# Optimization experiments

Measured on AMD Instinct MI355X. Metric: run time of the kernel, lower is better.

Reference implementation:

```python
import jax, jax.numpy as jnp
import numpy as np

N_SAMPLES = 131072
N_EVENTS = 128
N_ATOMS = 32
ATOM_SIZE = 512
LATENT_DIM = 16
TOTAL_LAYERS = 7  # log2(n_events)


def setup_inputs() -> dict:
    key = jax.random.key(0)
    ks = jax.random.split(key, 9)
    r = lambda k, s: jax.random.normal(k, s, dtype=jnp.float32) * 0.1
    return {
        "base_latent": r(ks[0], (1, LATENT_DIM)),
        "to_off_w": r(ks[1], (TOTAL_LAYERS, 2, LATENT_DIM)),
        "split_w": r(ks[2], (TOTAL_LAYERS, 2 * LATENT_DIM, LATENT_DIM)),
        "split_b": r(ks[3], (TOTAL_LAYERS, 2 * LATENT_DIM)),
        "atoms": r(ks[4], (N_ATOMS, ATOM_SIZE)),
        "to_atoms_w": r(ks[5], (N_ATOMS, LATENT_DIM)),
        "to_atoms_b": r(ks[6], (N_ATOMS,)),
        "to_amp_w": r(ks[7], (1, LATENT_DIM)),
        "to_amp_b": r(ks[8], (1,)),
    }


def fft_shift(a, shift):
    # FFT-based fractional delay: pad to 3*n, phase-rotate spectrum, crop.
    n = a.shape[-1]
    shift_samples = shift * n * 0.5  # shift: (B, E, 1)
    a = jnp.pad(a, [(0, 0)] * (a.ndim - 1) + [(0, n * 2)])
    spec = jnp.fft.rfft(a, axis=-1, norm="ortho")
    n_coeffs = spec.shape[-1]
    coeffs = (jnp.arange(n_coeffs) * 2j * jnp.pi) / n_coeffs  # (n_coeffs,)
    spec = spec * jnp.exp(coeffs * shift_samples)  # broadcast (B,E,n_coeffs)
    samples = jnp.fft.irfft(spec, axis=-1, norm="ortho")
    return samples[..., :n]


def _forward(base_latent, to_off_w, split_w, split_b, atoms,
             to_atoms_w, to_atoms_b, to_amp_w, to_amp_b):
    x = base_latent[:, None, :]                     # (1, 1, L)
    base_times = jnp.zeros((1, 1, 1), dtype=x.dtype)
    for i in range(TOTAL_LAYERS):
        scale = 1.0 / (2 ** i)
        b, e, _ = x.shape
        to = jax.nn.sigmoid(jnp.einsum("bel,ol->beo", x, to_off_w[i]))  # (b,e,2)
        base_times = (base_times + to * scale).reshape(b, e * 2, 1)
        split = jnp.einsum("bel,ol->beo", x, split_w[i]) + split_b[i]   # (b,e,2L)
        x = split.reshape(b, e * 2, LATENT_DIM)
    # x: (1, 128, L), base_times: (1, 128, 1)
    mix = jnp.einsum("bel,al->bea", x, to_atoms_w) + to_atoms_b          # (1,E,A)
    ev = jnp.einsum("bea,at->bet", mix, atoms)                           # (1,E,512)
    n_arr = jnp.arange(ATOM_SIZE, dtype=ev.dtype)
    window = 0.54 - 0.46 * jnp.cos(2.0 * jnp.pi * n_arr / ATOM_SIZE)     # periodic hamming
    ev = ev * window
    ev = jnp.pad(ev, ((0, 0), (0, 0), (0, N_SAMPLES - ATOM_SIZE)))       # (1,E,n_samples)
    ev = ev / (jnp.linalg.norm(ev, axis=-1, keepdims=True) + 1e-8)       # unit_norm
    amps = jnp.einsum("bel,ol->beo", x, to_amp_w) + to_amp_b             # (1,E,1)
    ev = ev * amps
    scheduled = fft_shift(ev, base_times)                                # (1,E,n_samples)
    return jnp.sum(scheduled, axis=1, keepdims=True)                     # (1,1,n_samples)


def reference(base_latent, to_off_w, split_w, split_b, atoms,
              to_atoms_w, to_atoms_b, to_amp_w, to_amp_b):
    return _forward(base_latent, to_off_w, split_w, split_b, atoms,
                    to_atoms_w, to_atoms_b, to_amp_w, to_amp_b)
```

## Files before the change

### kernel.cpp

```cpp
#include <hip/hip_runtime.h>
#include <hip/hip_bf16.h>
#include <math.h>

constexpr int NSAMP  = 131072;
constexpr int NEV    = 128;
constexpr int ASIZE  = 512;
constexpr int LDIM   = 16;
constexpr int NLAYER = 7;
constexpr int NFFT   = 393216;
constexpr int MHALF  = 196608;
constexpr int QN     = 65536;
constexpr double TWO_PI = 6.283185307179586;


__device__ __forceinline__ float2 cmulf(float2 a, float2 b) {
    return make_float2(a.x*b.x - a.y*b.y, a.x*b.y + a.y*b.x);
}
__device__ __forceinline__ float2 CADD(float2 a, float2 b){ return make_float2(a.x+b.x, a.y+b.y); }
__device__ __forceinline__ float2 CSUB(float2 a, float2 b){ return make_float2(a.x-b.x, a.y-b.y); }

__device__ __forceinline__ void phase_sc(float th32, float* ps, float* pc) {
    const double th = (double)th32;
    const double n  = rint(th * 0.15915494309189535);
    double r = fma(-n, 6.283185307179586, th);
    r = fma(-n, 2.4492935982947064e-16, r);
    __sincosf((float)r, ps, pc);
}

#define RT2 0.70710678118654752f
#define DFT8F(A0,A1,A2,A3,A4,A5,A6,A7, X0,X1,X2,X3,X4,X5,X6,X7) { \
  float2 b0=CADD(A0,A4), b1=CADD(A1,A5), b2=CADD(A2,A6), b3=CADD(A3,A7); \
  float2 c0=CSUB(A0,A4); \
  float2 d1=CSUB(A1,A5), d2=CSUB(A2,A6), d3=CSUB(A3,A7); \
  float2 c1=make_float2((d1.x+d1.y)*RT2, (d1.y-d1.x)*RT2); \
  float2 c2=make_float2(d2.y, -d2.x); \
  float2 c3=make_float2((d3.y-d3.x)*RT2, -(d3.x+d3.y)*RT2); \
  float2 t0=CADD(b0,b2), t1=CSUB(b0,b2), t2=CADD(b1,b3), t3=CSUB(b1,b3); \
  X0=CADD(t0,t2); X4=CSUB(t0,t2); \
  X2=make_float2(t1.x+t3.y, t1.y-t3.x); X6=make_float2(t1.x-t3.y, t1.y+t3.x); \
  t0=CADD(c0,c2); t1=CSUB(c0,c2); t2=CADD(c1,c3); t3=CSUB(c1,c3); \
  X1=CADD(t0,t2); X5=CSUB(t0,t2); \
  X3=make_float2(t1.x+t3.y, t1.y-t3.x); X7=make_float2(t1.x-t3.y, t1.y+t3.x); \
}

__global__ __launch_bounds__(256) void twiddles(
    double2* __restrict__ Tw256, double2* __restrict__ Tw512,
    double2* __restrict__ Tw768, double2* __restrict__ Tw64k)
{
    const int t = threadIdx.x;
    double s, c;
    sincos(TWO_PI*(double)t/256.0,   &s, &c); Tw256[t] = make_double2(c, s);
    sincos(TWO_PI*(double)t/512.0,   &s, &c); Tw512[t] = make_double2(c, s);
    sincos(TWO_PI*(double)t/768.0,   &s, &c); Tw768[t] = make_double2(c, s);
    sincos(TWO_PI*(double)t/65536.0, &s, &c); Tw64k[t] = make_double2(c, s);
}

__global__ __launch_bounds__(256) void tree_f32(
    const float* __restrict__ base, const float* __restrict__ to_off_w,
    const float* __restrict__ split_w, const float* __restrict__ split_b,
    float* __restrict__ xF, float* __restrict__ sF)
{
    __shared__ float xA[NEV*LDIM], xB[NEV*LDIM], bA[NEV], bB[NEV];
    const int tid = threadIdx.x;
    if (tid < LDIM) xA[tid] = base[tid];
    if (tid == 0) bA[0] = 0.0f;
    __syncthreads();
    float* xi = xA; float* xo = xB; float* bi = bA; float* bo = bB;
    for (int i = 0; i < NLAYER; ++i) {
        const int ein = 1 << i;
        const float scale = 1.0f / (float)(1 << i);
        for (int idx = tid; idx < ein*32; idx += 256) {
            const int ep = idx >> 5, o2 = idx & 31;
            const float* wr = split_w + (i*32 + o2)*LDIM;
            const float* xr = xi + ep*LDIM;
            float s = __fmul_rn(xr[0], wr[0]);
            for (int l = 1; l < LDIM; ++l)
                s = __fadd_rn(s, __fmul_rn(xr[l], wr[l]));
            s = __fadd_rn(s, split_b[i*32 + o2]);
            xo[(ep*2 + (o2>>4))*LDIM + (o2&15)] = s;
        }
        for (int idx = tid; idx < ein*2; idx += 256) {
            const int ep = idx >> 1, o = idx & 1;
            const float* wr = to_off_w + (i*2 + o)*LDIM;
            const float* xr = xi + ep*LDIM;
            float v = __fmul_rn(xr[0], wr[0]);
            for (int l = 1; l < LDIM; ++l)
                v = __fadd_rn(v, __fmul_rn(xr[l], wr[l]));
            const float ef = (float)exp(-(double)v);
            const float sg = __fdiv_rn(1.0f, __fadd_rn(1.0f, ef));
            bo[ep*2 + o] = __fadd_rn(bi[ep], __fmul_rn(sg, scale));
        }
        __syncthreads();
        float* t;
        t = xi; xi = xo; xo = t;
        t = bi; bi = bo; bo = t;
    }
    for (int idx = tid; idx < NEV*LDIM; idx += 256) xF[idx] = xi[idx];
    for (int e = tid; e < NEV; e += 256)
        sF[e] = __fmul_rn(__fmul_rn(bi[e], 131072.0f), 0.5f);
}

__global__ __launch_bounds__(256) void events_f32(
    const float* __restrict__ atoms, const float* __restrict__ to_atoms_w,
    const float* __restrict__ to_atoms_b, const float* __restrict__ to_amp_w,
    const float* __restrict__ to_amp_b, const float* __restrict__ xF,
    float* __restrict__ zf)
{
    const int e = blockIdx.x;
    const int tid = threadIdx.x;
    __shared__ float mixS[32];
    __shared__ float evS[ASIZE];
    __shared__ double red[256];
    __shared__ float scl[2];
    const float* x = xF + e*LDIM;
    if (tid < 32) {
        const float* wr = to_atoms_w + tid*LDIM;
        float m = __fmul_rn(x[0], wr[0]);
        for (int l = 1; l < LDIM; ++l) m = __fadd_rn(m, __fmul_rn(x[l], wr[l]));
        mixS[tid] = __fadd_rn(m, to_atoms_b[tid]);
    }
    __syncthreads();
    double ss = 0.0;
    for (int u = tid; u < ASIZE; u += 256) {
        float v = __fmul_rn(mixS[0], atoms[u]);
        for (int a = 1; a < 32; ++a)
            v = __fadd_rn(v, __fmul_rn(mixS[a], atoms[a*ASIZE + u]));
        const float ang = __fdiv_rn(__fmul_rn(6.283185307179586f, (float)u), 512.0f);
        const float cw = (float)cos((double)ang);
        const float w  = __fsub_rn(0.54f, __fmul_rn(0.46f, cw));
        v = __fmul_rn(v, w);
        evS[u] = v;
        ss += (double)v * (double)v;
    }
    red[tid] = ss; __syncthreads();
    for (int s = 128; s > 0; s >>= 1) { if (tid < s) red[tid] += red[tid+s]; __syncthreads(); }
    if (tid == 0) {
        const float nf = (float)sqrt(red[0]);
        scl[0] = __fadd_rn(nf, 1e-8f);
        float a = __fmul_rn(x[0], to_amp_w[0]);
        for (int l = 1; l < LDIM; ++l) a = __fadd_rn(a, __fmul_rn(x[l], to_amp_w[l]));
        scl[1] = __fadd_rn(a, to_amp_b[0]);
    }
    __syncthreads();
    const float den = scl[0], amp = scl[1];
    for (int u = tid; u < ASIZE; u += 256)
        zf[e*ASIZE + u] = __fmul_rn(__fdiv_rn(evS[u], den), amp);
}

__global__ __launch_bounds__(256, 4) void forward_reg8(
    const float* __restrict__ zf, const float* __restrict__ sF,
    float* __restrict__ Hqf)
{
    __shared__ float2 FB[4*576];
    __shared__ float2 T[512];
    __shared__ float2 W[448];
    __shared__ float  sSh[32];
    const int b       = blockIdx.x >> 2;
    const int quarter = blockIdx.x & 3;
    const int tid  = threadIdx.x;
    const int wave = tid >> 6, lane = tid & 63;
    float2* F = FB + wave*576;
    const int e0 = quarter*32;

    for (int j = tid; j < 512; j += 256) {
        double s1, c1;
        sincos(-TWO_PI*(double)(b*j)/(double)NFFT, &s1, &c1);
        T[j] = make_float2((float)c1, (float)s1);
        if (j < 448) {
            sincos(-TWO_PI*(double)j/512.0, &s1, &c1);
            W[j] = make_float2((float)c1, (float)s1);
        }
    }
    if (tid < 32) sSh[tid] = sF[e0 + tid];
    __syncthreads();

    float c2a[4], c2b[4];
    #pragma unroll
    for (int j = 0; j < 4; ++j) {
        const int a  = lane + 64*j;
        const int k1 = b + 768*a;
        const int k2 = (768 - b) + 768*(255 - a);
        c2a[j] = __fdiv_rn(__fmul_rn((float)(2*k1), 3.14159274101257324f), 196609.0f);
        c2b[j] = __fdiv_rn(__fmul_rn((float)(2*k2), 3.14159274101257324f), 196609.0f);
    }

    float a1R[4]={0,0,0,0}, a1I[4]={0,0,0,0};
    float a2R[4]={0,0,0,0}, a2I[4]={0,0,0,0};
    const int ph = lane + (lane >> 3);

    for (int it = 0; it < 8; ++it) {
        const int e = e0 + wave*8 + it;
        const float* zp = zf + e*ASIZE;
        {
            float2 i0,i1,i2,i3,i4,i5,i6,i7;
            {
                float z; float2 tt;
                z = zp[lane      ]; tt = T[lane      ]; i0 = make_float2(z*tt.x, z*tt.y);
                z = zp[lane +  64]; tt = T[lane +  64]; i1 = make_float2(z*tt.x, z*tt.y);
                z = zp[lane + 128]; tt = T[lane + 128]; i2 = make_float2(z*tt.x, z*tt.y);
                z = zp[lane + 192]; tt = T[lane + 192]; i3 = make_float2(z*tt.x, z*tt.y);
                z = zp[lane + 256]; tt = T[lane + 256]; i4 = make_float2(z*tt.x, z*tt.y);
                z = zp[lane + 320]; tt = T[lane + 320]; i5 = make_float2(z*tt.x, z*tt.y);
                z = zp[lane + 384]; tt = T[lane + 384]; i6 = make_float2(z*tt.x, z*tt.y);
                z = zp[lane + 448]; tt = T[lane + 448]; i7 = make_float2(z*tt.x, z*tt.y);
            }
            float2 x0,x1,x2,x3,x4,x5,x6,x7;
            DFT8F(i0,i1,i2,i3,i4,i5,i6,i7, x0,x1,x2,x3,x4,x5,x6,x7);
            const int ob = 9*lane;
            const float2 wb = W[lane];
            float2 wm = wb;
            F[ob]   = x0;
            F[ob+1] = cmulf(x1, wm); wm = cmulf(wm, wb);
            F[ob+2] = cmulf(x2, wm); wm = cmulf(wm, wb);
            F[ob+3] = cmulf(x3, wm); wm = cmulf(wm, wb);
            F[ob+4] = cmulf(x4, wm); wm = cmulf(wm, wb);
            F[ob+5] = cmulf(x5, wm); wm = cmulf(wm, wb);
            F[ob+6] = cmulf(x6, wm); wm = cmulf(wm, wb);
            F[ob+7] = cmulf(x7, wm);
        }
        {
            const float2 i0 = F[ph      ], i1 = F[ph +  72], i2 = F[ph + 144],
                         i3 = F[ph + 216], i4 = F[ph + 288], i5 = F[ph + 360],
                         i6 = F[ph + 432], i7 = F[ph + 504];
            float2 x0,x1,x2,x3,x4,x5,x6,x7;
            DFT8F(i0,i1,i2,i3,i4,i5,i6,i7, x0,x1,x2,x3,x4,x5,x6,x7);
            const int q = lane & 7, p = lane >> 3;
            const int ob = q + 72*p;
            const float2 wb = W[8*p];
            float2 wm = wb;
            F[ob]    = x0;
            F[ob+ 9] = cmulf(x1, wm); wm = cmulf(wm, wb);
            F[ob+18] = cmulf(x2, wm); wm = cmulf(wm, wb);
            F[ob+27] = cmulf(x3, wm); wm = cmulf(wm, wb);
            F[ob+36] = cmulf(x4, wm); wm = cmulf(wm, wb);
            F[ob+45] = cmulf(x5, wm); wm = cmulf(wm, wb);
            F[ob+54] = cmulf(x6, wm); wm = cmulf(wm, wb);
            F[ob+63] = cmulf(x7, wm);
        }
        float2 Y[8];
        {
            const float2 i0 = F[ph      ], i1 = F[ph +  72], i2 = F[ph + 144],
                         i3 = F[ph + 216], i4 = F[ph + 288], i5 = F[ph + 360],
                         i6 = F[ph + 432], i7 = F[ph + 504];
            DFT8F(i0,i1,i2,i3,i4,i5,i6,i7, Y[0],Y[1],Y[2],Y[3],Y[4],Y[5],Y[6],Y[7]);
        }
        const float se = sSh[wave*8 + it];
        #pragma unroll
        for (int j = 0; j < 4; ++j) {
            float ps, pc;
            const float2 S0 = Y[j];
            phase_sc(__fmul_rn(c2a[j], se), &ps, &pc);
            a1R[j] = fmaf(S0.x, pc, fmaf(-S0.y, ps, a1R[j]));
            a1I[j] = fmaf(S0.x, ps, fmaf( S0.y, pc, a1I[j]));
            const float2 S1 = Y[j+4];
            phase_sc(__fmul_rn(c2b[j], se), &ps, &pc);
            a2R[j] = fmaf(S1.x, pc, fmaf( S1.y, ps, a2R[j]));
            a2I[j] = fmaf(S1.x, ps, fmaf(-S1.y, pc, a2I[j]));
        }
    }

    float* redF = (float*)FB;
    #pragma unroll
    for (int round = 0; round < 2; ++round) {
        __syncthreads();
        const int j0 = 2*round;
        float* my = redF + (wave*64 + lane)*8;
        my[0]=a1R[j0];   my[1]=a1I[j0];   my[2]=a2R[j0];   my[3]=a2I[j0];
        my[4]=a1R[j0+1]; my[5]=a1I[j0+1]; my[6]=a2R[j0+1]; my[7]=a2I[j0+1];
        __syncthreads();
        const int s = tid >> 2, c = tid & 3;
        #pragma unroll
        for (int jr = 0; jr < 2; ++jr) {
            float v = 0.f;
            #pragma unroll
            for (int w = 0; w < 4; ++w) v += redF[(w*64 + s)*8 + jr*4 + c];
            const int as = s + 64*(j0 + jr);
            if (c < 2) {
                Hqf[2*(quarter*196609 + b*256 + as) + c] = v;
            } else if (b != 384) {
                if (b != 0)
                    Hqf[2*(quarter*196609 + (768-b)*256 + (255-as)) + (c-2)] = v;
                else if (as == 0)
                    Hqf[2*(quarter*196609 + 196608) + (c-2)] = v;
            }
        }
    }
}

__device__ __forceinline__ void ifft256_stage(
    const double2* __restrict__ src, double2* __restrict__ dst, int t, int s4,
    const double2* __restrict__ Tw256)
{
    const int lg = 2*s4, st = 1 << lg;
    const int q = t & (st-1), p = t >> lg;
    const double2 A0 = src[t], A1 = src[t+64], A2 = src[t+128], A3 = src[t+192];
    const double Pr = A0.x + A2.x, Pi_ = A0.y + A2.y;
    const double Qr = A0.x - A2.x, Qi  = A0.y - A2.y;
    const double Rr = A1.x + A3.x, Ri  = A1.y + A3.y;
    const double Sr = A1.x - A3.x, Si  = A1.y - A3.y;
    const int tw = p*st;
    const double2 w1 = Tw256[tw];
    const double2 w2 = Tw256[(2*tw) & 255];
    const double2 w3 = Tw256[(3*tw) & 255];
    const int o = q + 4*st*p;
    dst[o] = make_double2(Pr + Rr, Pi_ + Ri);
    const double u1r = Qr - Si, u1i = Qi + Sr;
    dst[o + st]   = make_double2(u1r*w1.x - u1i*w1.y, u1r*w1.y + u1i*w1.x);
    const double u2r = Pr - Rr, u2i = Pi_ - Ri;
    dst[o + 2*st] = make_double2(u2r*w2.x - u2i*w2.y, u2r*w2.y + u2i*w2.x);
    const double u3r = Qr + Si, u3i = Qi - Sr;
    dst[o + 3*st] = make_double2(u3r*w3.x - u3i*w3.y, u3r*w3.y + u3i*w3.x);
}

__global__ __launch_bounds__(256) void inv_a(
    const float* __restrict__ Hqf, const double2* __restrict__ Tw256,
    const double2* __restrict__ Tw512, const double2* __restrict__ Tw64k,
    float2* __restrict__ Yg)
{
    __shared__ double2 buf[4*512];
    const int tid = threadIdx.x;
    const int jj = tid >> 6, t = tid & 63;
    const int job = blockIdx.x*4 + jj;
    const int l = job >> 8, j1 = job & 255;
    const int k0 = 3*j1 + l;
    double2* A = buf + jj*512;
    double2* B = A + 256;
    const float2* Hq2 = (const float2*)Hqf;

    double Ss, Sc; sincos(TWO_PI*(double)k0/(double)NFFT, &Ss, &Sc);

    #pragma unroll
    for (int r = 0; r < 4; ++r) {
        const int j2 = t + 64*r;
        const int idxK = k0*256 + j2;
        int idxM;
        if (k0 > 0) idxM = (768 - k0)*256 + (255 - j2);
        else        idxM = (j2 == 0) ? 196608 : (256 - j2);
        double hkR=0, hkI=0, hmR=0, hmI=0;
        #pragma unroll
        for (int q = 0; q < 4; ++q) {
            const float2 vk = Hq2[q*196609 + idxK];
            const float2 vm = Hq2[q*196609 + idxM];
            hkR += (double)vk.x; hkI += (double)vk.y;
            hmR += (double)vm.x; hmI += (double)vm.y;
        }
        if (k0 == 0 && j2 == 0) { hkI = 0.0; hmI = 0.0; }
        const double Pr = hkR + hmR, Pi_ = hkI - hmI;
        const double Qr = hkR - hmR, Qi = hkI + hmI;
        const double2 t5 = Tw512[j2];
        const double Wc = Sc*t5.x - Ss*t5.y;
        const double Wsn = Sc*t5.y + Ss*t5.x;
        const double WQr = Wc*Qr - Wsn*Qi;
        const double WQi = Wc*Qi + Wsn*Qr;
        A[j2] = make_double2(0.5*(Pr - WQi), 0.5*(Pi_ + WQr));
    }

    ifft256_stage(A, B, t, 0, Tw256);
    ifft256_stage(B, A, t, 1, Tw256);
    ifft256_stage(A, B, t, 2, Tw256);
    ifft256_stage(B, A, t, 3, Tw256);

    #pragma unroll
    for (int r = 0; r < 4; ++r) {
        const int m1 = t + 64*r;
        const double2 v = A[m1];
        const int vv = j1*m1;
        const double2 wa = Tw256[vv >> 8];
        const double2 wb = Tw64k[vv & 255];
        const double twc = wa.x*wb.x - wa.y*wb.y;
        const double tws = wa.x*wb.y + wa.y*wb.x;
        Yg[job*256 + m1] = make_float2((float)(v.x*twc - v.y*tws),
                                       (float)(v.x*tws + v.y*twc));
    }
}

__global__ __launch_bounds__(256) void inv_b(
    const float2* __restrict__ Yg, const double2* __restrict__ Tw256,
    const double2* __restrict__ Tw768, float* __restrict__ out)
{
    __shared__ double2 buf[3*512];
    const int m1 = blockIdx.x;
    const int tid = threadIdx.x;
    const int l = tid >> 6, t = tid & 63;
    if (l < 3) {
        double2* A = buf + l*512;
        double2* B = A + 256;
        #pragma unroll
        for (int r = 0; r < 4; ++r) {
            const int j1 = t + 64*r;
            const float2 g = Yg[(l*256 + j1)*256 + m1];
            A[j1] = make_double2((double)g.x, (double)g.y);
        }
        ifft256_stage(A, B, t, 0, Tw256);
        ifft256_stage(B, A, t, 1, Tw256);
        ifft256_stage(A, B, t, 2, Tw256);
        ifft256_stage(B, A, t, 3, Tw256);
    }
    __syncthreads();

    const int m2 = tid;
    const double2 F0 = buf[0*512 + m2];
    const double2 F1 = buf[1*512 + m2];
    const double2 F2 = buf[2*512 + m2];
    double sm, cm; sincos(TWO_PI*(double)m1/(double)MHALF, &sm, &cm);
    const double2 t7 = Tw768[m2];
    const double w1c = cm*t7.x - sm*t7.y, w1s = cm*t7.y + sm*t7.x;
    const double w2c = w1c*w1c - w1s*w1s, w2s = 2.0*w1c*w1s;
    const double gr = F0.x + (w1c*F1.x - w1s*F1.y) + (w2c*F2.x - w2s*F2.y);
    const double gi = F0.y + (w1c*F1.y + w1s*F1.x) + (w2c*F2.y + w2s*F2.x);
    const int m = m1 + 256*m2;
    const double inv = 1.0/(double)MHALF;
    out[2*m]     = (float)(gr*inv);
    out[2*m + 1] = (float)(gi*inv);
}

extern "C" void kernel_launch(void* const* d_in, const int* in_sizes, int n_in,
                              void* d_out, int out_size, void* d_ws, size_t ws_size,
                              hipStream_t stream) {
    const float* base       = (const float*)d_in[0];
    const float* to_off_w   = (const float*)d_in[1];
    const float* split_w    = (const float*)d_in[2];
    const float* split_b    = (const float*)d_in[3];
    const float* atoms      = (const float*)d_in[4];
    const float* to_atoms_w = (const float*)d_in[5];
    const float* to_atoms_b = (const float*)d_in[6];
    const float* to_amp_w   = (const float*)d_in[7];
    const float* to_amp_b   = (const float*)d_in[8];
    float* out = (float*)d_out;

    char* ws = (char*)d_ws;
    double2* Tw256 = (double2*)(ws + 0);
    double2* Tw512 = (double2*)(ws + 4096);
    double2* Tw768 = (double2*)(ws + 8192);
    double2* Tw64k = (double2*)(ws + 12288);
    float*   sF    = (float*)(ws + 16384);
    float*   xF    = (float*)(ws + 16896);
    float*   zf    = (float*)(ws + 25088);
    float*   Hqf   = (float*)(ws + 287232);
    float2*  Yg    = (float2*)(ws + 6578720);

    twiddles<<<1, 256, 0, stream>>>(Tw256, Tw512, Tw768, Tw64k);
    tree_f32<<<1, 256, 0, stream>>>(base, to_off_w, split_w, split_b, xF, sF);
    events_f32<<<NEV, 256, 0, stream>>>(atoms, to_atoms_w, to_atoms_b,
                                        to_amp_w, to_amp_b, xF, zf);
    forward_reg8<<<385*4, 256, 0, stream>>>(zf, sF, Hqf);
    inv_a<<<192, 256, 0, stream>>>(Hqf, Tw256, Tw512, Tw64k, Yg);
    inv_b<<<256, 256, 0, stream>>>(Yg, Tw256, Tw768, out);
}
```

Baseline: 146.4 us.

## Merge init kernels, precompute phase tables, switch inverse FFT to fp32

Merges the twiddle and tree kernels into one multi-block init kernel that also precomputes the per-bin phase tables in global memory, so the forward kernel no longer evaluates double-precision sincos per block. The forward kernel derives its radix-8 base twiddles with __sincosf, drops its shared tables and lowers its occupancy hint. The inverse FFT kernels move from double to float arithmetic and float twiddle tables. Work is regrouped into one 64-thread block per job, the intermediate is stored transposed for contiguous reads, and the Yg buffer aliases the phase-table region. Accuracy of the large inverse FFT may drop.

```diff
diff --git a/kernel.cpp b/kernel.cpp
--- a/kernel.cpp
+++ b/kernel.cpp
@@ -9,7 +9,6 @@
 constexpr int NLAYER = 7;
 constexpr int NFFT   = 393216;
 constexpr int MHALF  = 196608;
-constexpr int QN     = 65536;
 constexpr double TWO_PI = 6.283185307179586;
 
 
@@ -43,61 +42,68 @@
   X3=make_float2(t1.x+t3.y, t1.y-t3.x); X7=make_float2(t1.x-t3.y, t1.y+t3.x); \
 }
 
-__global__ __launch_bounds__(256) void twiddles(
-    double2* __restrict__ Tw256, double2* __restrict__ Tw512,
-    double2* __restrict__ Tw768, double2* __restrict__ Tw64k)
-{
-    const int t = threadIdx.x;
-    double s, c;
-    sincos(TWO_PI*(double)t/256.0,   &s, &c); Tw256[t] = make_double2(c, s);
-    sincos(TWO_PI*(double)t/512.0,   &s, &c); Tw512[t] = make_double2(c, s);
-    sincos(TWO_PI*(double)t/768.0,   &s, &c); Tw768[t] = make_double2(c, s);
-    sincos(TWO_PI*(double)t/65536.0, &s, &c); Tw64k[t] = make_double2(c, s);
-}
-
-__global__ __launch_bounds__(256) void tree_f32(
+__global__ __launch_bounds__(256) void init_all(
     const float* __restrict__ base, const float* __restrict__ to_off_w,
     const float* __restrict__ split_w, const float* __restrict__ split_b,
-    float* __restrict__ xF, float* __restrict__ sF)
-{
-    __shared__ float xA[NEV*LDIM], xB[NEV*LDIM], bA[NEV], bB[NEV];
+    float* __restrict__ xF, float* __restrict__ sF,
+    float2* __restrict__ Twf, float2* __restrict__ Ttab)
+{
+    const int blk = blockIdx.x;
     const int tid = threadIdx.x;
-    if (tid < LDIM) xA[tid] = base[tid];
-    if (tid == 0) bA[0] = 0.0f;
-    __syncthreads();
-    float* xi = xA; float* xo = xB; float* bi = bA; float* bo = bB;
-    for (int i = 0; i < NLAYER; ++i) {
-        const int ein = 1 << i;
-        const float scale = 1.0f / (float)(1 << i);
-        for (int idx = tid; idx < ein*32; idx += 256) {
-            const int ep = idx >> 5, o2 = idx & 31;
-            const float* wr = split_w + (i*32 + o2)*LDIM;
-            const float* xr = xi + ep*LDIM;
-            float s = __fmul_rn(xr[0], wr[0]);
-            for (int l = 1; l < LDIM; ++l)
-                s = __fadd_rn(s, __fmul_rn(xr[l], wr[l]));
-            s = __fadd_rn(s, split_b[i*32 + o2]);
-            xo[(ep*2 + (o2>>4))*LDIM + (o2&15)] = s;
-        }
-        for (int idx = tid; idx < ein*2; idx += 256) {
-            const int ep = idx >> 1, o = idx & 1;
-            const float* wr = to_off_w + (i*2 + o)*LDIM;
-            const float* xr = xi + ep*LDIM;
-            float v = __fmul_rn(xr[0], wr[0]);
-            for (int l = 1; l < LDIM; ++l)
-                v = __fadd_rn(v, __fmul_rn(xr[l], wr[l]));
-            const float ef = (float)exp(-(double)v);
-            const float sg = __fdiv_rn(1.0f, __fadd_rn(1.0f, ef));
-            bo[ep*2 + o] = __fadd_rn(bi[ep], __fmul_rn(sg, scale));
-        }
+    if (blk == 0) {
+        __shared__ float xA[NEV*LDIM], xB[NEV*LDIM], bA[NEV], bB[NEV];
+        if (tid < LDIM) xA[tid] = base[tid];
+        if (tid == 0) bA[0] = 0.0f;
         __syncthreads();
-        float* t;
-        t = xi; xi = xo; xo = t;
-        t = bi; bi = bo; bo = t;
-    }
-    for (int idx = tid; idx < NEV*LDIM; idx += 256) xF[idx] = xi[idx];
-    for (int e = tid; e < NEV; e += 256)
-        sF[e] = __fmul_rn(__fmul_rn(bi[e], 131072.0f), 0.5f);
+        float* xi = xA; float* xo = xB; float* bi = bA; float* bo = bB;
+        for (int i = 0; i < NLAYER; ++i) {
+            const int ein = 1 << i;
+            const float scale = 1.0f / (float)(1 << i);
+            for (int idx = tid; idx < ein*32; idx += 256) {
+                const int ep = idx >> 5, o2 = idx & 31;
+                const float* wr = split_w + (i*32 + o2)*LDIM;
+                const float* xr = xi + ep*LDIM;
+                float s = __fmul_rn(xr[0], wr[0]);
+                for (int l = 1; l < LDIM; ++l)
+                    s = __fadd_rn(s, __fmul_rn(xr[l], wr[l]));
+                s = __fadd_rn(s, split_b[i*32 + o2]);
+                xo[(ep*2 + (o2>>4))*LDIM + (o2&15)] = s;
+            }
+            for (int idx = tid; idx < ein*2; idx += 256) {
+                const int ep = idx >> 1, o = idx & 1;
+                const float* wr = to_off_w + (i*2 + o)*LDIM;
+                const float* xr = xi + ep*LDIM;
+                float v = __fmul_rn(xr[0], wr[0]);
+                for (int l = 1; l < LDIM; ++l)
+                    v = __fadd_rn(v, __fmul_rn(xr[l], wr[l]));
+                const float ef = (float)exp(-(double)v);
+                const float sg = __fdiv_rn(1.0f, __fadd_rn(1.0f, ef));
+                bo[ep*2 + o] = __fadd_rn(bi[ep], __fmul_rn(sg, scale));
+            }
+            __syncthreads();
+            float* t;
+            t = xi; xi = xo; xo = t;
+            t = bi; bi = bo; bo = t;
+        }
+        for (int idx = tid; idx < NEV*LDIM; idx += 256) xF[idx] = xi[idx];
+        for (int e = tid; e < NEV; e += 256)
+            sF[e] = __fmul_rn(__fmul_rn(bi[e], 131072.0f), 0.5f);
+        return;
+    }
+    if (blk == 1) {
+        double s, c;
+        sincos(TWO_PI*(double)tid/256.0,   &s, &c); Twf[tid]       = make_float2((float)c,(float)s);
+        sincos(TWO_PI*(double)tid/512.0,   &s, &c); Twf[256 + tid] = make_float2((float)c,(float)s);
+        sincos(TWO_PI*(double)tid/768.0,   &s, &c); Twf[512 + tid] = make_float2((float)c,(float)s);
+        sincos(TWO_PI*(double)tid/65536.0, &s, &c); Twf[768 + tid] = make_float2((float)c,(float)s);
+        return;
+    }
+    const int b = blk - 2;
+    for (int j = tid; j < 512; j += 256) {
+        double s, c;
+        sincos(-TWO_PI*(double)(b*j)/(double)NFFT, &s, &c);
+        Ttab[b*512 + j] = make_float2((float)c, (float)s);
+    }
 }
 
 __global__ __launch_bounds__(256) void events_f32(
@@ -147,13 +153,11 @@
         zf[e*ASIZE + u] = __fmul_rn(__fdiv_rn(evS[u], den), amp);
 }
 
-__global__ __launch_bounds__(256, 4) void forward_reg8(
+__global__ __launch_bounds__(256, 3) void forward_v2(
     const float* __restrict__ zf, const float* __restrict__ sF,
-    float* __restrict__ Hqf)
+    const float2* __restrict__ Ttab, float* __restrict__ Hqf)
 {
     __shared__ float2 FB[4*576];
-    __shared__ float2 T[512];
-    __shared__ float2 W[448];
     __shared__ float  sSh[32];
     const int b       = blockIdx.x >> 2;
     const int quarter = blockIdx.x & 3;
@@ -161,18 +165,14 @@
     const int wave = tid >> 6, lane = tid & 63;
     float2* F = FB + wave*576;
     const int e0 = quarter*32;
-
-    for (int j = tid; j < 512; j += 256) {
-        double s1, c1;
-        sincos(-TWO_PI*(double)(b*j)/(double)NFFT, &s1, &c1);
-        T[j] = make_float2((float)c1, (float)s1);
-        if (j < 448) {
-            sincos(-TWO_PI*(double)j/512.0, &s1, &c1);
-            W[j] = make_float2((float)c1, (float)s1);
-        }
-    }
+    const float2* Tg = Ttab + b*512;
+
     if (tid < 32) sSh[tid] = sF[e0 + tid];
     __syncthreads();
+
+    float2 w0b, w1b;
+    __sincosf(-6.283185307179586f/512.0f * (float)lane,        &w0b.y, &w0b.x);
+    __sincosf(-6.283185307179586f/64.0f  * (float)(lane >> 3), &w1b.y, &w1b.x);
 
     float c2a[4], c2b[4];
     #pragma unroll
@@ -195,27 +195,26 @@
             float2 i0,i1,i2,i3,i4,i5,i6,i7;
             {
                 float z; float2 tt;
-                z = zp[lane      ]; tt = T[lane      ]; i0 = make_float2(z*tt.x, z*tt.y);
-                z = zp[lane +  64]; tt = T[lane +  64]; i1 = make_float2(z*tt.x, z*tt.y);
-                z = zp[lane + 128]; tt = T[lane + 128]; i2 = make_float2(z*tt.x, z*tt.y);
-                z = zp[lane + 192]; tt = T[lane + 192]; i3 = make_float2(z*tt.x, z*tt.y);
-                z = zp[lane + 256]; tt = T[lane + 256]; i4 = make_float2(z*tt.x, z*tt.y);
-                z = zp[lane + 320]; tt = T[lane + 320]; i5 = make_float2(z*tt.x, z*tt.y);
-                z = zp[lane + 384]; tt = T[lane + 384]; i6 = make_float2(z*tt.x, z*tt.y);
-                z = zp[lane + 448]; tt = T[lane + 448]; i7 = make_float2(z*tt.x, z*tt.y);
+                z = zp[lane      ]; tt = Tg[lane      ]; i0 = make_float2(z*tt.x, z*tt.y);
+                z = zp[lane +  64]; tt = Tg[lane +  64]; i1 = make_float2(z*tt.x, z*tt.y);
+                z = zp[lane + 128]; tt = Tg[lane + 128]; i2 = make_float2(z*tt.x, z*tt.y);
+                z = zp[lane + 192]; tt = Tg[lane + 192]; i3 = make_float2(z*tt.x, z*tt.y);
+                z = zp[lane + 256]; tt = Tg[lane + 256]; i4 = make_float2(z*tt.x, z*tt.y);
+                z = zp[lane + 320]; tt = Tg[lane + 320]; i5 = make_float2(z*tt.x, z*tt.y);
+                z = zp[lane + 384]; tt = Tg[lane + 384]; i6 = make_float2(z*tt.x, z*tt.y);
+                z = zp[lane + 448]; tt = Tg[lane + 448]; i7 = make_float2(z*tt.x, z*tt.y);
             }
             float2 x0,x1,x2,x3,x4,x5,x6,x7;
             DFT8F(i0,i1,i2,i3,i4,i5,i6,i7, x0,x1,x2,x3,x4,x5,x6,x7);
             const int ob = 9*lane;
-            const float2 wb = W[lane];
-            float2 wm = wb;
+            float2 wm = w0b;
             F[ob]   = x0;
-            F[ob+1] = cmulf(x1, wm); wm = cmulf(wm, wb);
-            F[ob+2] = cmulf(x2, wm); wm = cmulf(wm, wb);
-            F[ob+3] = cmulf(x3, wm); wm = cmulf(wm, wb);
-            F[ob+4] = cmulf(x4, wm); wm = cmulf(wm, wb);
-            F[ob+5] = cmulf(x5, wm); wm = cmulf(wm, wb);
-            F[ob+6] = cmulf(x6, wm); wm = cmulf(wm, wb);
+            F[ob+1] = cmulf(x1, wm); wm = cmulf(wm, w0b);
+            F[ob+2] = cmulf(x2, wm); wm = cmulf(wm, w0b);
+            F[ob+3] = cmulf(x3, wm); wm = cmulf(wm, w0b);
+            F[ob+4] = cmulf(x4, wm); wm = cmulf(wm, w0b);
+            F[ob+5] = cmulf(x5, wm); wm = cmulf(wm, w0b);
+            F[ob+6] = cmulf(x6, wm); wm = cmulf(wm, w0b);
             F[ob+7] = cmulf(x7, wm);
         }
         {
@@ -226,15 +225,14 @@
             DFT8F(i0,i1,i2,i3,i4,i5,i6,i7, x0,x1,x2,x3,x4,x5,x6,x7);
             const int q = lane & 7, p = lane >> 3;
             const int ob = q + 72*p;
-            const float2 wb = W[8*p];
-            float2 wm = wb;
+            float2 wm = w1b;
             F[ob]    = x0;
-            F[ob+ 9] = cmulf(x1, wm); wm = cmulf(wm, wb);
-            F[ob+18] = cmulf(x2, wm); wm = cmulf(wm, wb);
-            F[ob+27] = cmulf(x3, wm); wm = cmulf(wm, wb);
-            F[ob+36] = cmulf(x4, wm); wm = cmulf(wm, wb);
-            F[ob+45] = cmulf(x5, wm); wm = cmulf(wm, wb);
-            F[ob+54] = cmulf(x6, wm); wm = cmulf(wm, wb);
+            F[ob+ 9] = cmulf(x1, wm); wm = cmulf(wm, w1b);
+            F[ob+18] = cmulf(x2, wm); wm = cmulf(wm, w1b);
+            F[ob+27] = cmulf(x3, wm); wm = cmulf(wm, w1b);
+            F[ob+36] = cmulf(x4, wm); wm = cmulf(wm, w1b);
+            F[ob+45] = cmulf(x5, wm); wm = cmulf(wm, w1b);
+            F[ob+54] = cmulf(x6, wm); wm = cmulf(wm, w1b);
             F[ob+63] = cmulf(x7, wm);
         }
         float2 Y[8];
@@ -287,47 +285,48 @@
     }
 }
 
-__device__ __forceinline__ void ifft256_stage(
-    const double2* __restrict__ src, double2* __restrict__ dst, int t, int s4,
-    const double2* __restrict__ Tw256)
+__device__ __forceinline__ void ifft256f_stage(
+    const float2* __restrict__ src, float2* __restrict__ dst, int t, int s4,
+    const float2* __restrict__ Tw256f)
 {
     const int lg = 2*s4, st = 1 << lg;
     const int q = t & (st-1), p = t >> lg;
-    const double2 A0 = src[t], A1 = src[t+64], A2 = src[t+128], A3 = src[t+192];
-    const double Pr = A0.x + A2.x, Pi_ = A0.y + A2.y;
-    const double Qr = A0.x - A2.x, Qi  = A0.y - A2.y;
-    const double Rr = A1.x + A3.x, Ri  = A1.y + A3.y;
-    const double Sr = A1.x - A3.x, Si  = A1.y - A3.y;
+    const float2 A0 = src[t], A1 = src[t+64], A2 = src[t+128], A3 = src[t+192];
+    const float Pr = A0.x + A2.x, Pi_ = A0.y + A2.y;
+    const float Qr = A0.x - A2.x, Qi  = A0.y - A2.y;
+    const float Rr = A1.x + A3.x, Ri  = A1.y + A3.y;
+    const float Sr = A1.x - A3.x, Si  = A1.y - A3.y;
     const int tw = p*st;
-    const double2 w1 = Tw256[tw];
-    const double2 w2 = Tw256[(2*tw) & 255];
-    const double2 w3 = Tw256[(3*tw) & 255];
+    const float2 w1 = Tw256f[tw];
+    const float2 w2 = Tw256f[(2*tw) & 255];
+    const float2 w3 = Tw256f[(3*tw) & 255];
     const int o = q + 4*st*p;
-    dst[o] = make_double2(Pr + Rr, Pi_ + Ri);
-    const double u1r = Qr - Si, u1i = Qi + Sr;
-    dst[o + st]   = make_double2(u1r*w1.x - u1i*w1.y, u1r*w1.y + u1i*w1.x);
-    const double u2r = Pr - Rr, u2i = Pi_ - Ri;
-    dst[o + 2*st] = make_double2(u2r*w2.x - u2i*w2.y, u2r*w2.y + u2i*w2.x);
-    const double u3r = Qr + Si, u3i = Qi - Sr;
-    dst[o + 3*st] = make_double2(u3r*w3.x - u3i*w3.y, u3r*w3.y + u3i*w3.x);
-}
-
-__global__ __launch_bounds__(256) void inv_a(
-    const float* __restrict__ Hqf, const double2* __restrict__ Tw256,
-    const double2* __restrict__ Tw512, const double2* __restrict__ Tw64k,
+    dst[o] = make_float2(Pr + Rr, Pi_ + Ri);
+    const float u1r = Qr - Si, u1i = Qi + Sr;
+    dst[o + st]   = make_float2(u1r*w1.x - u1i*w1.y, u1r*w1.y + u1i*w1.x);
+    const float u2r = Pr - Rr, u2i = Pi_ - Ri;
+    dst[o + 2*st] = make_float2(u2r*w2.x - u2i*w2.y, u2r*w2.y + u2i*w2.x);
+    const float u3r = Qr + Si, u3i = Qi - Sr;
+    dst[o + 3*st] = make_float2(u3r*w3.x - u3i*w3.y, u3r*w3.y + u3i*w3.x);
+}
+
+__global__ __launch_bounds__(64) void inv_a(
+    const float* __restrict__ Hqf, const float2* __restrict__ Twf,
     float2* __restrict__ Yg)
 {
-    __shared__ double2 buf[4*512];
-    const int tid = threadIdx.x;
-    const int jj = tid >> 6, t = tid & 63;
-    const int job = blockIdx.x*4 + jj;
+    __shared__ float2 buf[512];
+    const int t = threadIdx.x;
+    const int job = blockIdx.x;
     const int l = job >> 8, j1 = job & 255;
     const int k0 = 3*j1 + l;
-    double2* A = buf + jj*512;
-    double2* B = A + 256;
+    float2* A = buf; float2* B = buf + 256;
     const float2* Hq2 = (const float2*)Hqf;
+    const float2* Tw256f = Twf;
+    const float2* Tw512f = Twf + 256;
+    const float2* Tw64kf = Twf + 768;
 
     double Ss, Sc; sincos(TWO_PI*(double)k0/(double)NFFT, &Ss, &Sc);
+    const float Scf = (float)Sc, Ssf = (float)Ss;
 
     #pragma unroll
     for (int r = 0; r < 4; ++r) {
@@ -336,82 +335,84 @@
         int idxM;
         if (k0 > 0) idxM = (768 - k0)*256 + (255 - j2);
         else        idxM = (j2 == 0) ? 196608 : (256 - j2);
-        double hkR=0, hkI=0, hmR=0, hmI=0;
+        float hkR=0.f, hkI=0.f, hmR=0.f, hmI=0.f;
         #pragma unroll
         for (int q = 0; q < 4; ++q) {
             const float2 vk = Hq2[q*196609 + idxK];
             const float2 vm = Hq2[q*196609 + idxM];
-            hkR += (double)vk.x; hkI += (double)vk.y;
-            hmR += (double)vm.x; hmI += (double)vm.y;
-        }
-        if (k0 == 0 && j2 == 0) { hkI = 0.0; hmI = 0.0; }
-        const double Pr = hkR + hmR, Pi_ = hkI - hmI;
-        const double Qr = hkR - hmR, Qi = hkI + hmI;
-        const double2 t5 = Tw512[j2];
-        const double Wc = Sc*t5.x - Ss*t5.y;
-        const double Wsn = Sc*t5.y + Ss*t5.x;
-        const double WQr = Wc*Qr - Wsn*Qi;
-        const double WQi = Wc*Qi + Wsn*Qr;
-        A[j2] = make_double2(0.5*(Pr - WQi), 0.5*(Pi_ + WQr));
-    }
-
-    ifft256_stage(A, B, t, 0, Tw256);
-    ifft256_stage(B, A, t, 1, Tw256);
-    ifft256_stage(A, B, t, 2, Tw256);
-    ifft256_stage(B, A, t, 3, Tw256);
+            hkR += vk.x; hkI += vk.y;
+            hmR += vm.x; hmI += vm.y;
+        }
+        if (k0 == 0 && j2 == 0) { hkI = 0.f; hmI = 0.f; }
+        const float Pr = hkR + hmR, Pi_ = hkI - hmI;
+        const float Qr = hkR - hmR, Qi = hkI + hmI;
+        const float2 t5 = Tw512f[j2];
+        const float Wc = Scf*t5.x - Ssf*t5.y;
+        const float Wsn = Scf*t5.y + Ssf*t5.x;
+        const float WQr = Wc*Qr - Wsn*Qi;
+        const float WQi = Wc*Qi + Wsn*Qr;
+        A[j2] = make_float2(0.5f*(Pr - WQi), 0.5f*(Pi_ + WQr));
+    }
+
+    ifft256f_stage(A, B, t, 0, Tw256f);
+    ifft256f_stage(B, A, t, 1, Tw256f);
+    ifft256f_stage(A, B, t, 2, Tw256f);
+    ifft256f_stage(B, A, t, 3, Tw256f);
 
     #pragma unroll
     for (int r = 0; r < 4; ++r) {
         const int m1 = t + 64*r;
-        const double2 v = A[m1];
+        const float2 v = A[m1];
         const int vv = j1*m1;
-        const double2 wa = Tw256[vv >> 8];
-        const double2 wb = Tw64k[vv & 255];
-        const double twc = wa.x*wb.x - wa.y*wb.y;
-        const double tws = wa.x*wb.y + wa.y*wb.x;
-        Yg[job*256 + m1] = make_float2((float)(v.x*twc - v.y*tws),
-                                       (float)(v.x*tws + v.y*twc));
-    }
-}
-
-__global__ __launch_bounds__(256) void inv_b(
-    const float2* __restrict__ Yg, const double2* __restrict__ Tw256,
-    const double2* __restrict__ Tw768, float* __restrict__ out)
-{
-    __shared__ double2 buf[3*512];
+        const float2 wa = Tw256f[vv >> 8];
+        const float2 wb = Tw64kf[vv & 255];
+        const float twc = wa.x*wb.x - wa.y*wb.y;
+        const float tws = wa.x*wb.y + wa.y*wb.x;
+        Yg[m1*768 + job] = make_float2(v.x*twc - v.y*tws, v.x*tws + v.y*twc);
+    }
+}
+
+__global__ __launch_bounds__(192) void inv_b(
+    const float2* __restrict__ Yg, const float2* __restrict__ Twf,
+    float* __restrict__ out)
+{
+    __shared__ float2 buf[3*512];
     const int m1 = blockIdx.x;
     const int tid = threadIdx.x;
     const int l = tid >> 6, t = tid & 63;
-    if (l < 3) {
-        double2* A = buf + l*512;
-        double2* B = A + 256;
+    const float2* Tw256f = Twf;
+    const float2* Tw768f = Twf + 512;
+    {
+        float2* A = buf + l*512;
+        float2* B = A + 256;
         #pragma unroll
         for (int r = 0; r < 4; ++r) {
             const int j1 = t + 64*r;
-            const float2 g = Yg[(l*256 + j1)*256 + m1];
-            A[j1] = make_double2((double)g.x, (double)g.y);
-        }
-        ifft256_stage(A, B, t, 0, Tw256);
-        ifft256_stage(B, A, t, 1, Tw256);
-        ifft256_stage(A, B, t, 2, Tw256);
-        ifft256_stage(B, A, t, 3, Tw256);
+            A[j1] = Yg[m1*768 + l*256 + j1];
+        }
+        ifft256f_stage(A, B, t, 0, Tw256f);
+        ifft256f_stage(B, A, t, 1, Tw256f);
+        ifft256f_stage(A, B, t, 2, Tw256f);
+        ifft256f_stage(B, A, t, 3, Tw256f);
     }
     __syncthreads();
 
-    const int m2 = tid;
-    const double2 F0 = buf[0*512 + m2];
-    const double2 F1 = buf[1*512 + m2];
-    const double2 F2 = buf[2*512 + m2];
-    double sm, cm; sincos(TWO_PI*(double)m1/(double)MHALF, &sm, &cm);
-    const double2 t7 = Tw768[m2];
-    const double w1c = cm*t7.x - sm*t7.y, w1s = cm*t7.y + sm*t7.x;
-    const double w2c = w1c*w1c - w1s*w1s, w2s = 2.0*w1c*w1s;
-    const double gr = F0.x + (w1c*F1.x - w1s*F1.y) + (w2c*F2.x - w2s*F2.y);
-    const double gi = F0.y + (w1c*F1.y + w1s*F1.x) + (w2c*F2.y + w2s*F2.x);
-    const int m = m1 + 256*m2;
-    const double inv = 1.0/(double)MHALF;
-    out[2*m]     = (float)(gr*inv);
-    out[2*m + 1] = (float)(gi*inv);
+    double smd, cmd; sincos(TWO_PI*(double)m1/(double)MHALF, &smd, &cmd);
+    const float cm = (float)cmd, sm = (float)smd;
+    const float inv = 1.0f/(float)MHALF;
+    for (int m2 = tid; m2 < 256; m2 += 192) {
+        const float2 F0 = buf[m2];
+        const float2 F1 = buf[512 + m2];
+        const float2 F2 = buf[1024 + m2];
+        const float2 t7 = Tw768f[m2];
+        const float w1c = cm*t7.x - sm*t7.y, w1s = cm*t7.y + sm*t7.x;
+        const float w2c = w1c*w1c - w1s*w1s, w2s = 2.0f*w1c*w1s;
+        const float gr = F0.x + (w1c*F1.x - w1s*F1.y) + (w2c*F2.x - w2s*F2.y);
+        const float gi = F0.y + (w1c*F1.y + w1s*F1.x) + (w2c*F2.y + w2s*F2.x);
+        const int m = m1 + 256*m2;
+        out[2*m]     = gr*inv;
+        out[2*m + 1] = gi*inv;
+    }
 }
 
 extern "C" void kernel_launch(void* const* d_in, const int* in_sizes, int n_in,
@@ -429,21 +430,19 @@
     float* out = (float*)d_out;
 
     char* ws = (char*)d_ws;
-    double2* Tw256 = (double2*)(ws + 0);
-    double2* Tw512 = (double2*)(ws + 4096);
-    double2* Tw768 = (double2*)(ws + 8192);
-    double2* Tw64k = (double2*)(ws + 12288);
-    float*   sF    = (float*)(ws + 16384);
-    float*   xF    = (float*)(ws + 16896);
-    float*   zf    = (float*)(ws + 25088);
-    float*   Hqf   = (float*)(ws + 287232);
-    float2*  Yg    = (float2*)(ws + 6578720);
-
-    twiddles<<<1, 256, 0, stream>>>(Tw256, Tw512, Tw768, Tw64k);
-    tree_f32<<<1, 256, 0, stream>>>(base, to_off_w, split_w, split_b, xF, sF);
+    float2* Twf  = (float2*)(ws + 0);
+    float*  sF   = (float*)(ws + 8192);
+    float*  xF   = (float*)(ws + 8704);
+    float*  zf   = (float*)(ws + 16896);
+    float2* Ttab = (float2*)(ws + 279040);
+    float2* Yg   = (float2*)(ws + 279040);
+    float*  Hqf  = (float*)(ws + 1856000);
+
+    init_all<<<387, 256, 0, stream>>>(base, to_off_w, split_w, split_b,
+                                      xF, sF, Twf, Ttab);
     events_f32<<<NEV, 256, 0, stream>>>(atoms, to_atoms_w, to_atoms_b,
                                         to_amp_w, to_amp_b, xF, zf);
-    forward_reg8<<<385*4, 256, 0, stream>>>(zf, sF, Hqf);
-    inv_a<<<192, 256, 0, stream>>>(Hqf, Tw256, Tw512, Tw64k, Yg);
-    inv_b<<<256, 256, 0, stream>>>(Yg, Tw256, Tw768, out);
-}
+    forward_v2<<<385*4, 256, 0, stream>>>(zf, sF, Ttab, Hqf);
+    inv_a<<<768, 64, 0, stream>>>(Hqf, Twf, Yg);
+    inv_b<<<256, 192, 0, stream>>>(Yg, Twf, out);
+}
```

New measurement: 138.3 us. 1.06x faster.
